# Kernel tuning notes

Hardware: AMD Instinct MI355X
Metric: run time of the kernel (lower is better)

The kernel has to match this reference:

```python
import jax, jax.numpy as jnp
import numpy as np

COMMITMENT_COST = 0.25


def setup_inputs() -> dict:
    key = jax.random.key(0)
    k1, k2 = jax.random.split(key)
    B, D, H, W = 64, 64, 32, 32
    K = 512
    x = jax.random.normal(k1, (B, D, H, W), dtype=jnp.float32)
    # torch init: uniform_(-1/K, 1/K)
    codebook = jax.random.uniform(k2, (K, D), dtype=jnp.float32,
                                  minval=-1.0 / K, maxval=1.0 / K)
    return {"x": x, "codebook": codebook}


def reference(x, codebook):
    B, D, H, W = x.shape
    K = codebook.shape[0]
    in_re = jnp.transpose(x, (0, 2, 3, 1))          # [B,H,W,D]
    flat = in_re.reshape(-1, D)                      # [N,D], N=B*H*W
    dist = (jnp.sum(flat * flat, axis=1, keepdims=True)
            + jnp.sum(codebook * codebook, axis=1)
            - 2.0 * jnp.matmul(flat, codebook.T))    # [N,K]
    idx = jnp.argmin(dist, axis=1)                   # [N]
    encoding = jax.nn.one_hot(idx, K, dtype=jnp.float32)  # [N,K]
    softmax_histogram = jnp.sum(jax.nn.softmax(-dist, axis=-1).reshape(B, -1, K), axis=1)  # [B,K]
    quantized = jnp.matmul(encoding, codebook).reshape(in_re.shape)  # [B,H,W,D]
    e_latent_loss = jnp.mean((jax.lax.stop_gradient(quantized) - in_re) ** 2)
    q_latent_loss = jnp.mean((quantized - jax.lax.stop_gradient(in_re)) ** 2)
    loss = q_latent_loss + COMMITMENT_COST * e_latent_loss
    # straight-through estimator
    quant_st = in_re + jax.lax.stop_gradient(quantized - in_re)
    avg_probs = jnp.mean(encoding, axis=0)
    perplexity = jnp.exp(-jnp.sum(avg_probs * jnp.log(avg_probs + 1e-10)))
    quant_out = jnp.transpose(quant_st, (0, 3, 1, 2))  # back to NCHW
    encoding_indice = idx.reshape(B, -1)               # [B, H*W]
    # per-batch histogram of code usage == sum of one-hots over spatial dim
    index_program = jnp.sum(encoding.reshape(B, -1, K), axis=1)  # [B,K]
    return (quant_out, loss, perplexity, encoding_indice, index_program, softmax_histogram)
```

## Files before the change

kernel.cpp:

```cpp
#include <hip/hip_runtime.h>


#define OFF_LOSS 4194304
#define OFF_PERP 4194305
#define OFF_ENC  4194306
#define OFF_IP   4259842
#define OFF_SH   4292610

#define WS_CBT   0
#define WS_CE2   32768
#define WS_SHP   33280
#define WS_LOSS  557568


typedef float f16v __attribute__((ext_vector_type(16)));

typedef __attribute__((address_space(1))) const void g_void;
typedef __attribute__((address_space(3))) void lds_void;
#define GLOAD_LDS(G, S) \
    __builtin_amdgcn_global_load_lds((g_void*)(G), (lds_void*)(S), 16, 0, 0)

__global__ __launch_bounds__(256) void vq_prep(const float* __restrict__ cb,
                                               float* __restrict__ ws)
{
    const int t  = blockIdx.x * 256 + threadIdx.x;
    const int kg = t >> 4;
    const int j  = t & 15;
    const float4 v = ((const float4*)cb)[(kg << 4) + j];
    float pr = v.x * v.x + v.y * v.y + v.z * v.z + v.w * v.w;
    #pragma unroll
    for (int off = 1; off < 16; off <<= 1) pr += __shfl_xor(pr, off, 16);
    if (j == 0) ws[WS_CE2 + kg] = pr;
    const int kc = kg >> 7, kl = kg & 127;
    float* base = ws + WS_CBT + (kc << 13) + (j << 9) + kl;
    base[0]   = v.x;
    base[128] = v.y;
    base[256] = v.z;
    base[384] = v.w;
}

#define FMA4(ACC, AV, K4) \
    ACC[(K4) + 0] = fmaf((AV), bq.x, ACC[(K4) + 0]); \
    ACC[(K4) + 1] = fmaf((AV), bq.y, ACC[(K4) + 1]); \
    ACC[(K4) + 2] = fmaf((AV), bq.z, ACC[(K4) + 2]); \
    ACC[(K4) + 3] = fmaf((AV), bq.w, ACC[(K4) + 3]);

#define FMA_CHUNK(KC) do { \
    const float4 bq = *(const float4*)&csT[((KC) << 13) + (d << 7) + (tc << 2)]; \
    FMA4(acc0, a0.x, (KC) << 2) \
    FMA4(acc1, a0.y, (KC) << 2) \
    FMA4(acc2, a0.z, (KC) << 2) \
    FMA4(acc3, a0.w, (KC) << 2) \
    FMA4(acc4, a1.x, (KC) << 2) \
    FMA4(acc5, a1.y, (KC) << 2) \
    FMA4(acc6, a1.z, (KC) << 2) \
    FMA4(acc7, a1.w, (KC) << 2) \
} while (0)

#define EPI_C(C, ACC) { \
    const int k = (((C) >> 2) << 7) + (tc << 2) + ((C) & 3); \
    const float t1 = xxr + ce2[k]; \
    const float dist = t1 - 2.f * ACC[C]; \
    ACC[C] = dist; \
    if (dist < m) { m = dist; bk = k; } }

#define EXP_C(C, ACC) { \
    const float e = __expf(m - ACC[C]); \
    ACC[C] = e; z += e; }

#define ROW_EPI(I, ACC, INVZ) do { \
    const int row = (tr << 3) + (I); \
    const float xxr = sxx[row]; \
    float m = 1e30f; int bk = 0; \
    EPI_C(0, ACC)  EPI_C(1, ACC)  EPI_C(2, ACC)  EPI_C(3, ACC) \
    EPI_C(4, ACC)  EPI_C(5, ACC)  EPI_C(6, ACC)  EPI_C(7, ACC) \
    EPI_C(8, ACC)  EPI_C(9, ACC)  EPI_C(10, ACC) EPI_C(11, ACC) \
    EPI_C(12, ACC) EPI_C(13, ACC) EPI_C(14, ACC) EPI_C(15, ACC) \
    _Pragma("unroll") \
    for (int off = 1; off < 32; off <<= 1) { \
        const float mo = __shfl_xor(m, off, 32); \
        const int   ko = __shfl_xor(bk, off, 32); \
        if (mo < m || (mo == m && ko < bk)) { m = mo; bk = ko; } \
    } \
    float z = 0.f; \
    EXP_C(0, ACC)  EXP_C(1, ACC)  EXP_C(2, ACC)  EXP_C(3, ACC) \
    EXP_C(4, ACC)  EXP_C(5, ACC)  EXP_C(6, ACC)  EXP_C(7, ACC) \
    EXP_C(8, ACC)  EXP_C(9, ACC)  EXP_C(10, ACC) EXP_C(11, ACC) \
    EXP_C(12, ACC) EXP_C(13, ACC) EXP_C(14, ACC) EXP_C(15, ACC) \
    _Pragma("unroll") \
    for (int off = 1; off < 32; off <<= 1) z += __shfl_xor(z, off, 32); \
    INVZ = 1.f / z; \
    if (tc == 0) { \
        sidx[row] = bk; \
        enc[((size_t)b << 10) + row0 + row] = (float)bk; \
    } \
} while (0)

#define HIST_C(C) { \
    const int k = (((C) >> 2) << 7) + (tc << 2) + ((C) & 3); \
    float cs = 0.f; \
    cs += acc0[C] * invz0; cs += acc1[C] * invz1; \
    cs += acc2[C] * invz2; cs += acc3[C] * invz3; \
    cs += acc4[C] * invz4; cs += acc5[C] * invz5; \
    cs += acc6[C] * invz6; cs += acc7[C] * invz7; \
    atomicAdd(&shist[k], cs); }

__global__ __launch_bounds__(256, 1) void vq_main(
    const float* __restrict__ x, const float* __restrict__ cb,
    const float* __restrict__ wsc,
    float* __restrict__ wso,
    float* __restrict__ out)
{
    __shared__ float  csT[4 * 64 * 128];
    __shared__ float  xs[64 * 64];
    __shared__ float  ce2[512];
    __shared__ float  sxx[64];
    __shared__ int    sidx[64];

    const int t    = threadIdx.x;
    const int blk  = blockIdx.x;
    const int b    = blk >> 4;
    const int row0 = (blk & 15) << 6;
    const int tr   = t >> 5;
    const int tc   = t & 31;

    const float4* cbT4 = (const float4*)(wsc + WS_CBT);
    float4* csT4 = (float4*)csT;

    {
        const float4* xb4 = (const float4*)(x + ((size_t)b << 16) + row0);
        #pragma unroll
        for (int p = 0; p < 4; ++p) {
            const int fi = (p << 8) + t;
            const int d  = fi >> 4;
            const int r4 = fi & 15;
            GLOAD_LDS(&xb4[(d << 8) + r4], &xs[(d << 6) + (r4 << 2)]);
        }
        #pragma unroll
        for (int q = 0; q < 32; ++q)
            GLOAD_LDS(&cbT4[(q << 8) + t], &csT4[(q << 8) + t]);
    }
    if (t < 128) ((float4*)ce2)[t] = ((const float4*)(wsc + WS_CE2))[t];

    __syncthreads();

    if (t < 64) {
        float s = 0.f;
        for (int d = 0; d < 64; ++d) { const float v = xs[(d << 6) + t]; s = fmaf(v, v, s); }
        sxx[t] = s;
    }

    f16v acc0 = 0.f, acc1 = 0.f, acc2 = 0.f, acc3 = 0.f;
    f16v acc4 = 0.f, acc5 = 0.f, acc6 = 0.f, acc7 = 0.f;

    #pragma unroll 4
    for (int d = 0; d < 64; ++d) {
        const float4 a0 = *(const float4*)&xs[(d << 6) + (tr << 3)];
        const float4 a1 = *(const float4*)&xs[(d << 6) + (tr << 3) + 4];
        FMA_CHUNK(0);
        FMA_CHUNK(1);
        FMA_CHUNK(2);
        FMA_CHUNK(3);
    }

    __syncthreads();

    float* enc = out + OFF_ENC;
    float invz0, invz1, invz2, invz3, invz4, invz5, invz6, invz7;
    ROW_EPI(0, acc0, invz0);
    ROW_EPI(1, acc1, invz1);
    ROW_EPI(2, acc2, invz2);
    ROW_EPI(3, acc3, invz3);
    ROW_EPI(4, acc4, invz4);
    ROW_EPI(5, acc5, invz5);
    ROW_EPI(6, acc6, invz6);
    ROW_EPI(7, acc7, invz7);

    __syncthreads();

    float* shist = csT;
    shist[t] = 0.f; shist[t + 256] = 0.f;
    __syncthreads();
    HIST_C(0)  HIST_C(1)  HIST_C(2)  HIST_C(3)
    HIST_C(4)  HIST_C(5)  HIST_C(6)  HIST_C(7)
    HIST_C(8)  HIST_C(9)  HIST_C(10) HIST_C(11)
    HIST_C(12) HIST_C(13) HIST_C(14) HIST_C(15)
    __syncthreads();
    {
        float* wsh = wso + WS_SHP + ((size_t)blk << 9);
        wsh[t]       = shist[t];
        wsh[t + 256] = shist[t + 256];
    }

    const int r4 = (t & 15) << 2;
    const int dq = t >> 4;
    const int c0 = sidx[r4], c1 = sidx[r4 + 1], c2 = sidx[r4 + 2], c3 = sidx[r4 + 3];
    float lsum = 0.f;
    #pragma unroll
    for (int p = 0; p < 4; ++p) {
        const int d = (p << 4) + dq;
        float4 q;
        q.x = cb[(c0 << 6) + d];
        q.y = cb[(c1 << 6) + d];
        q.z = cb[(c2 << 6) + d];
        q.w = cb[(c3 << 6) + d];
        const float4 xv = *(const float4*)&xs[(d << 6) + r4];
        const float d0 = q.x - xv.x, d1 = q.y - xv.y, d2 = q.z - xv.z, d3 = q.w - xv.w;
        lsum = fmaf(d0, d0, lsum); lsum = fmaf(d1, d1, lsum);
        lsum = fmaf(d2, d2, lsum); lsum = fmaf(d3, d3, lsum);
        *(float4*)&out[(((size_t)(b << 6) + d) << 10) + row0 + r4] = q;
    }
    #pragma unroll
    for (int off = 1; off < 64; off <<= 1) lsum += __shfl_xor(lsum, off, 64);
    if ((t & 63) == 0) wso[WS_LOSS + (blk << 2) + (t >> 6)] = lsum;
}

__global__ __launch_bounds__(512) void vq_reduce(const float* __restrict__ ws,
                                                 float* __restrict__ out)
{
    __shared__ int hist[512];
    const int b = blockIdx.x, t = threadIdx.x;
    const float* p = ws + WS_SHP + ((size_t)b << 13) + t;
    float s = 0.f;
    #pragma unroll
    for (int j = 0; j < 16; ++j) s += p[j << 9];
    out[OFF_SH + (b << 9) + t] = s;
    hist[t] = 0;
    __syncthreads();
    const float* enc = out + OFF_ENC + ((size_t)b << 10);
    const int ca = (int)enc[t];
    const int cbn = (int)enc[t + 512];
    atomicAdd(&hist[ca], 1);
    atomicAdd(&hist[cbn], 1);
    __syncthreads();
    out[OFF_IP + (b << 9) + t] = (float)hist[t];
}

__global__ __launch_bounds__(512) void vq_final(const float* __restrict__ ws,
                                                float* __restrict__ out)
{
    __shared__ float red[8], red2[8];
    const int t = threadIdx.x;
    const float* ip = out + OFF_IP;
    float c0 = 0.f, c1 = 0.f, c2 = 0.f, c3 = 0.f;
    #pragma unroll
    for (int bb = 0; bb < 64; bb += 4) {
        c0 += ip[((bb + 0) << 9) + t];
        c1 += ip[((bb + 1) << 9) + t];
        c2 += ip[((bb + 2) << 9) + t];
        c3 += ip[((bb + 3) << 9) + t];
    }
    const float c = (c0 + c1) + (c2 + c3);
    const float pav = c * (1.0f / 65536.f);
    float h = pav * logf(pav + 1e-10f);
    const float* wl = ws + WS_LOSS;
    float ls = 0.f;
    #pragma unroll
    for (int j = 0; j < 8; ++j) ls += wl[(j << 9) + t];
    #pragma unroll
    for (int off = 1; off < 64; off <<= 1) {
        h  += __shfl_xor(h, off, 64);
        ls += __shfl_xor(ls, off, 64);
    }
    if ((t & 63) == 0) { red[t >> 6] = h; red2[t >> 6] = ls; }
    __syncthreads();
    if (t == 0) {
        float H = 0.f, L = 0.f;
        #pragma unroll
        for (int w = 0; w < 8; ++w) { H += red[w]; L += red2[w]; }
        out[OFF_PERP] = expf(-H);
        out[OFF_LOSS] = L * (1.25f / 4194304.f);
    }
}

extern "C" void kernel_launch(void* const* d_in, const int* in_sizes, int n_in,
                              void* d_out, int out_size, void* d_ws, size_t ws_size,
                              hipStream_t stream)
{
    const float* x  = (const float*)d_in[0];
    const float* cb = (const float*)d_in[1];
    float* out = (float*)d_out;
    float* ws  = (float*)d_ws;
    (void)ws_size;

    vq_prep  <<<32,   256, 0, stream>>>(cb, ws);
    vq_main  <<<1024, 256, 0, stream>>>(x, cb, ws, ws, out);
    vq_reduce<<<64,   512, 0, stream>>>(ws, out);
    vq_final <<<1,    512, 0, stream>>>(ws, out);
}
```

Measured before the change: 189.3 us.

## Double-buffer codebook staging in LDS and fuse reduce/final via last-block counter

```diff
diff --git a/kernel.cpp b/kernel.cpp
--- a/kernel.cpp
+++ b/kernel.cpp
@@ -11,6 +11,7 @@
 #define WS_CE2   32768
 #define WS_SHP   33280
 #define WS_LOSS  557568
+#define WS_CNT   561664
 
 
 typedef float f16v __attribute__((ext_vector_type(16)));
@@ -23,6 +24,9 @@
 __global__ __launch_bounds__(256) void vq_prep(const float* __restrict__ cb,
                                                float* __restrict__ ws)
 {
+    if (blockIdx.x == 0 && threadIdx.x == 0)
+        ((int*)ws)[WS_CNT] = 0;
+
     const int t  = blockIdx.x * 256 + threadIdx.x;
     const int kg = t >> 4;
     const int j  = t & 15;
@@ -45,16 +49,33 @@
     ACC[(K4) + 2] = fmaf((AV), bq.z, ACC[(K4) + 2]); \
     ACC[(K4) + 3] = fmaf((AV), bq.w, ACC[(K4) + 3]);
 
-#define FMA_CHUNK(KC) do { \
-    const float4 bq = *(const float4*)&csT[((KC) << 13) + (d << 7) + (tc << 2)]; \
-    FMA4(acc0, a0.x, (KC) << 2) \
-    FMA4(acc1, a0.y, (KC) << 2) \
-    FMA4(acc2, a0.z, (KC) << 2) \
-    FMA4(acc3, a0.w, (KC) << 2) \
-    FMA4(acc4, a1.x, (KC) << 2) \
-    FMA4(acc5, a1.y, (KC) << 2) \
-    FMA4(acc6, a1.z, (KC) << 2) \
-    FMA4(acc7, a1.w, (KC) << 2) \
+#define STAGE_SEG(S, BUF4) do { \
+    GLOAD_LDS(&cbT4[((S) << 10) + t],       &BUF4[t]); \
+    GLOAD_LDS(&cbT4[((S) << 10) + 256 + t], &BUF4[256 + t]); \
+    GLOAD_LDS(&cbT4[((S) << 10) + 512 + t], &BUF4[512 + t]); \
+    GLOAD_LDS(&cbT4[((S) << 10) + 768 + t], &BUF4[768 + t]); \
+} while (0)
+
+#define COMPUTE_SEG(KC, H, BUF) do { \
+    _Pragma("unroll 2") \
+    for (int db = 0; db < 8; ++db) { \
+        const float* cbase = &BUF[(db << 9) + (tc << 2)]; \
+        _Pragma("unroll") \
+        for (int j = 0; j < 4; ++j) { \
+            const int d = ((H) << 5) + (db << 2) + j; \
+            const float4 a0 = *(const float4*)&xs[(d << 6) + (tr << 3)]; \
+            const float4 a1 = *(const float4*)&xs[(d << 6) + (tr << 3) + 4]; \
+            const float4 bq = *(const float4*)&cbase[j << 7]; \
+            FMA4(acc0, a0.x, (KC) << 2) \
+            FMA4(acc1, a0.y, (KC) << 2) \
+            FMA4(acc2, a0.z, (KC) << 2) \
+            FMA4(acc3, a0.w, (KC) << 2) \
+            FMA4(acc4, a1.x, (KC) << 2) \
+            FMA4(acc5, a1.y, (KC) << 2) \
+            FMA4(acc6, a1.z, (KC) << 2) \
+            FMA4(acc7, a1.w, (KC) << 2) \
+        } \
+    } \
 } while (0)
 
 #define EPI_C(C, ACC) { \
@@ -111,8 +132,9 @@
     float* __restrict__ wso,
     float* __restrict__ out)
 {
-    __shared__ float  csT[4 * 64 * 128];
     __shared__ float  xs[64 * 64];
+    __shared__ float  cs0[32 * 128];
+    __shared__ float  cs1[32 * 128];
     __shared__ float  ce2[512];
     __shared__ float  sxx[64];
     __shared__ int    sidx[64];
@@ -125,7 +147,8 @@
     const int tc   = t & 31;
 
     const float4* cbT4 = (const float4*)(wsc + WS_CBT);
-    float4* csT4 = (float4*)csT;
+    float4* cs0_4 = (float4*)cs0;
+    float4* cs1_4 = (float4*)cs1;
 
     {
         const float4* xb4 = (const float4*)(x + ((size_t)b << 16) + row0);
@@ -136,10 +159,8 @@
             const int r4 = fi & 15;
             GLOAD_LDS(&xb4[(d << 8) + r4], &xs[(d << 6) + (r4 << 2)]);
         }
-        #pragma unroll
-        for (int q = 0; q < 32; ++q)
-            GLOAD_LDS(&cbT4[(q << 8) + t], &csT4[(q << 8) + t]);
-    }
+    }
+    STAGE_SEG(0, cs0_4);
     if (t < 128) ((float4*)ce2)[t] = ((const float4*)(wsc + WS_CE2))[t];
 
     __syncthreads();
@@ -153,17 +174,14 @@
     f16v acc0 = 0.f, acc1 = 0.f, acc2 = 0.f, acc3 = 0.f;
     f16v acc4 = 0.f, acc5 = 0.f, acc6 = 0.f, acc7 = 0.f;
 
-    #pragma unroll 4
-    for (int d = 0; d < 64; ++d) {
-        const float4 a0 = *(const float4*)&xs[(d << 6) + (tr << 3)];
-        const float4 a1 = *(const float4*)&xs[(d << 6) + (tr << 3) + 4];
-        FMA_CHUNK(0);
-        FMA_CHUNK(1);
-        FMA_CHUNK(2);
-        FMA_CHUNK(3);
-    }
-
-    __syncthreads();
+    STAGE_SEG(1, cs1_4);  COMPUTE_SEG(0, 0, cs0);  __syncthreads();
+    STAGE_SEG(2, cs0_4);  COMPUTE_SEG(0, 1, cs1);  __syncthreads();
+    STAGE_SEG(3, cs1_4);  COMPUTE_SEG(1, 0, cs0);  __syncthreads();
+    STAGE_SEG(4, cs0_4);  COMPUTE_SEG(1, 1, cs1);  __syncthreads();
+    STAGE_SEG(5, cs1_4);  COMPUTE_SEG(2, 0, cs0);  __syncthreads();
+    STAGE_SEG(6, cs0_4);  COMPUTE_SEG(2, 1, cs1);  __syncthreads();
+    STAGE_SEG(7, cs1_4);  COMPUTE_SEG(3, 0, cs0);  __syncthreads();
+    COMPUTE_SEG(3, 1, cs1);
 
     float* enc = out + OFF_ENC;
     float invz0, invz1, invz2, invz3, invz4, invz5, invz6, invz7;
@@ -178,7 +196,7 @@
 
     __syncthreads();
 
-    float* shist = csT;
+    float* shist = cs0;
     shist[t] = 0.f; shist[t + 256] = 0.f;
     __syncthreads();
     HIST_C(0)  HIST_C(1)  HIST_C(2)  HIST_C(3)
@@ -215,10 +233,11 @@
     if ((t & 63) == 0) wso[WS_LOSS + (blk << 2) + (t >> 6)] = lsum;
 }
 
-__global__ __launch_bounds__(512) void vq_reduce(const float* __restrict__ ws,
-                                                 float* __restrict__ out)
+__global__ __launch_bounds__(512) void vq_tail(float* __restrict__ ws,
+                                               float* __restrict__ out)
 {
     __shared__ int hist[512];
+    __shared__ int s_last;
     const int b = blockIdx.x, t = threadIdx.x;
     const float* p = ws + WS_SHP + ((size_t)b << 13) + t;
     float s = 0.f;
@@ -228,19 +247,20 @@
     hist[t] = 0;
     __syncthreads();
     const float* enc = out + OFF_ENC + ((size_t)b << 10);
-    const int ca = (int)enc[t];
+    const int ca  = (int)enc[t];
     const int cbn = (int)enc[t + 512];
     atomicAdd(&hist[ca], 1);
     atomicAdd(&hist[cbn], 1);
     __syncthreads();
     out[OFF_IP + (b << 9) + t] = (float)hist[t];
-}
-
-__global__ __launch_bounds__(512) void vq_final(const float* __restrict__ ws,
-                                                float* __restrict__ out)
-{
+
+    __threadfence();
+    if (t == 0) s_last = (atomicAdd(&((int*)ws)[WS_CNT], 1) == 63);
+    __syncthreads();
+    if (!s_last) return;
+    __threadfence();
+
     __shared__ float red[8], red2[8];
-    const int t = threadIdx.x;
     const float* ip = out + OFF_IP;
     float c0 = 0.f, c1 = 0.f, c2 = 0.f, c3 = 0.f;
     #pragma unroll
@@ -283,8 +303,7 @@
     float* ws  = (float*)d_ws;
     (void)ws_size;
 
-    vq_prep  <<<32,   256, 0, stream>>>(cb, ws);
-    vq_main  <<<1024, 256, 0, stream>>>(x, cb, ws, ws, out);
-    vq_reduce<<<64,   512, 0, stream>>>(ws, out);
-    vq_final <<<1,    512, 0, stream>>>(ws, out);
+    vq_prep <<<32,   256, 0, stream>>>(cb, ws);
+    vq_main <<<1024, 256, 0, stream>>>(x, cb, ws, ws, out);
+    vq_tail <<<64,   512, 0, stream>>>(ws, out);
 }
```

Result: slower. 216.1 us (+14.2%).
